# Kernel tuning notes

Measured on AMD Instinct MI355X. Metric: run time of the kernel, lower is better.

## Reference

```python
import jax, jax.numpy as jnp
import numpy as np

HID = 2048      # hidden_size
H = 16          # num query heads
KV = 4          # num kv heads
HD = HID // H   # head_dim = 128
THETA = 1000000.0
T = 2048        # tokens (single causal sequence)


def _rope(x, positions):
    # neox-style rotate-half RoPE over full head_dim. x: [T, h, HD]
    half = HD // 2
    inv_freq = THETA ** (-jnp.arange(half, dtype=jnp.float32) * 2.0 / HD)  # [half]
    freqs = positions.astype(jnp.float32)[:, None] * inv_freq              # [T, half]
    cos = jnp.cos(freqs)[:, None, :]
    sin = jnp.sin(freqs)[:, None, :]
    x1, x2 = x[..., :half], x[..., half:]
    return jnp.concatenate([x1 * cos - x2 * sin, x2 * cos + x1 * sin], axis=-1)


def setup_inputs() -> dict:
    key = jax.random.key(0)
    k1, k2, k3 = jax.random.split(key, 3)
    hidden_states = jax.random.normal(k1, (T, HID), jnp.float32) * 0.02
    w_qkv = jax.random.normal(k2, (HID, (H + 2 * KV) * HD), jnp.float32) * 0.02
    w_o = jax.random.normal(k3, (H * HD, HID), jnp.float32) * 0.02
    positions = jnp.arange(T, dtype=jnp.int32)
    return {"hidden_states": hidden_states, "w_qkv": w_qkv, "w_o": w_o,
            "positions": positions}


def reference(hidden_states, w_qkv, w_o, positions):
    q_size, kv_size = H * HD, KV * HD
    qkv = hidden_states @ w_qkv                                  # [T, q+2kv]
    q = qkv[:, :q_size].reshape(T, H, HD)
    k = qkv[:, q_size:q_size + kv_size].reshape(T, KV, HD)
    v = qkv[:, q_size + kv_size:].reshape(T, KV, HD)
    q = _rope(q, positions)
    k = _rope(k, positions)
    # GQA: expand kv heads to query heads
    group = H // KV
    k_e = jnp.repeat(k, group, axis=1)                           # [T, H, HD]
    v_e = jnp.repeat(v, group, axis=1)
    scale = HD ** -0.5
    scores = jnp.einsum('thd,shd->hts', q, k_e) * scale          # [H, T, T]
    causal = positions[:, None] >= positions[None, :]            # [T, T]
    scores = jnp.where(causal[None, :, :], scores, -1e30)
    attn = jax.nn.softmax(scores, axis=-1)
    o = jnp.einsum('hts,shd->thd', attn, v_e).reshape(T, H * HD)
    return o @ w_o
```

## Files before the change

### kernel.cpp

```cpp
#include <hip/hip_runtime.h>
#include <hip/hip_bf16.h>

#define T_LEN 2048
#define HID 2048
#define NH 16
#define NKV 4
#define HD 128
#define QKV_COLS 3072

typedef __attribute__((ext_vector_type(8))) short bf16x8;
typedef __attribute__((ext_vector_type(4))) float f32x4;

static __device__ __forceinline__ ushort f2bf(float f) {
  __hip_bfloat16 h = __float2bfloat16(f);
  return *reinterpret_cast<ushort*>(&h);
}
static __device__ __forceinline__ float bf2f(ushort u) {
  union { unsigned int i; float f; } v;
  v.i = ((unsigned int)u) << 16;
  return v.f;
}

static __device__ __forceinline__ void async_copy16(const ushort* g, ushort* l) {
  __builtin_amdgcn_global_load_lds(
      (const __attribute__((address_space(1))) unsigned int*)g,
      (__attribute__((address_space(3))) unsigned int*)l, 16, 0, 0);
}

__global__ __launch_bounds__(256) void prep(
    const float* __restrict__ hidden, ushort* __restrict__ hb,
    const float* __restrict__ w_qkv, ushort* __restrict__ wqkvT,
    const int* __restrict__ positions, float2* __restrict__ tbl,
    const float* __restrict__ w_o, ushort* __restrict__ woT) {
  __shared__ float t[64][65];
  const int b = blockIdx.x;
  const int tid = threadIdx.x;
  if (b < 4096) {
    int idx = (b * 256 + tid) * 4;
    float4 v = *(const float4*)(hidden + idx);
    ushort4 o;
    o.x = f2bf(v.x); o.y = f2bf(v.y); o.z = f2bf(v.z); o.w = f2bf(v.w);
    *(ushort4*)(hb + idx) = o;
  } else if (b < 5632) {
    const int tb = b - 4096;
    const int bk = (tb & 31) * 64, bn = (tb >> 5) * 64;
    const int c = tid & 63;
#pragma unroll
    for (int i = 0; i < 16; ++i) {
      int r = (tid >> 6) + i * 4;
      t[r][c] = w_qkv[(size_t)(bk + r) * QKV_COLS + bn + c];
    }
    __syncthreads();
#pragma unroll
    for (int i = 0; i < 16; ++i) {
      int r = (tid >> 6) + i * 4;
      wqkvT[(size_t)(bn + r) * HID + bk + c] = f2bf(t[c][r]);
    }
  } else if (b < 6144) {
    const int rb = b - 5632;
    const int tt = rb * 4 + (tid >> 6), j = tid & 63;
    double inv_freq = pow(1000000.0, -(double)(2 * j) / 128.0);
    double ang = (double)positions[tt] * inv_freq;
    double s, c2;
    sincos(ang, &s, &c2);
    tbl[(size_t)tt * 64 + j] = make_float2((float)c2, (float)s);
  } else {
    const int tb = b - 6144;
    const int bk = (tb & 31) * 64, bn = (tb >> 5) * 64;
    const int c = tid & 63;
#pragma unroll
    for (int i = 0; i < 16; ++i) {
      int r = (tid >> 6) + i * 4;
      t[r][c] = w_o[(size_t)(bk + r) * HID + bn + c];
    }
    __syncthreads();
#pragma unroll
    for (int i = 0; i < 16; ++i) {
      int r = (tid >> 6) + i * 4;
      woT[(size_t)(bn + r) * HID + bk + c] = f2bf(t[c][r]);
    }
  }
}

__global__ __launch_bounds__(256) void transpose_cast(
    const float* __restrict__ W, ushort* __restrict__ WT, int K, int N) {
  __shared__ float t[64][65];
  const int bk = blockIdx.x * 64, bn = blockIdx.y * 64;
  const int tid = threadIdx.x;
  const int c = tid & 63;
#pragma unroll
  for (int i = 0; i < 16; ++i) {
    int r = (tid >> 6) + i * 4;
    t[r][c] = W[(size_t)(bk + r) * N + bn + c];
  }
  __syncthreads();
#pragma unroll
  for (int i = 0; i < 16; ++i) {
    int r = (tid >> 6) + i * 4;
    WT[(size_t)(bn + r) * K + bk + c] = f2bf(t[c][r]);
  }
}

template <bool OUT_BF16>
__global__ __launch_bounds__(256, 3) void gemm_bt(
    const ushort* __restrict__ A, const ushort* __restrict__ BT,
    void* __restrict__ C, int M, int N, int K) {
  __shared__ __align__(16) ushort lds[2][1536 * 8];
  const int tid = threadIdx.x;
  const int bm = blockIdx.y * 64, bn = blockIdx.x * 128;
  const int wave = tid >> 6, lane = tid & 63;
  const int lr = lane & 15, lq = lane >> 4;
  const int wm = (wave & 1) * 32, wn = (wave >> 1) * 64;

  f32x4 acc[2][4];
#pragma unroll
  for (int i = 0; i < 2; ++i)
#pragma unroll
    for (int j = 0; j < 4; ++j) {
      acc[i][j][0] = 0.f; acc[i][j][1] = 0.f;
      acc[i][j][2] = 0.f; acc[i][j][3] = 0.f;
    }

  auto stage = [&](int k0, int buf) {
#pragma unroll
    for (int it = 0; it < 2; ++it) {
      int c = it * 256 + tid;
      int row = c >> 3, sl = c & 7, kc = sl ^ (row & 7);
      async_copy16(A + (size_t)(bm + row) * K + k0 + kc * 8, &lds[buf][c * 8]);
    }
#pragma unroll
    for (int it = 0; it < 4; ++it) {
      int c = it * 256 + tid;
      int row = c >> 3, sl = c & 7, kc = sl ^ (row & 7);
      async_copy16(BT + (size_t)(bn + row) * K + k0 + kc * 8,
                   &lds[buf][(512 + c) * 8]);
    }
  };

  stage(0, 0);
  __syncthreads();
  int cur = 0;
  for (int k0 = 0; k0 < K; k0 += 64) {
    if (k0 + 64 < K) stage(k0 + 64, cur ^ 1);
#pragma unroll
    for (int ks = 0; ks < 2; ++ks) {
      bf16x8 af[2], bfr[4];
#pragma unroll
      for (int mi = 0; mi < 2; ++mi) {
        int row = wm + mi * 16 + lr, kc = ks * 4 + lq;
        af[mi] = *(const bf16x8*)&lds[cur][(row * 8 + (kc ^ (row & 7))) * 8];
      }
#pragma unroll
      for (int ni = 0; ni < 4; ++ni) {
        int row = wn + ni * 16 + lr, kc = ks * 4 + lq;
        bfr[ni] =
            *(const bf16x8*)&lds[cur][(512 + row * 8 + (kc ^ (row & 7))) * 8];
      }
#pragma unroll
      for (int mi = 0; mi < 2; ++mi)
#pragma unroll
        for (int ni = 0; ni < 4; ++ni)
          acc[mi][ni] = __builtin_amdgcn_mfma_f32_16x16x32_bf16(
              af[mi], bfr[ni], acc[mi][ni], 0, 0, 0);
    }
    __syncthreads();
    cur ^= 1;
  }

#pragma unroll
  for (int mi = 0; mi < 2; ++mi)
#pragma unroll
    for (int ni = 0; ni < 4; ++ni)
#pragma unroll
      for (int r = 0; r < 4; ++r) {
        size_t row = bm + wm + mi * 16 + lq * 4 + r;
        size_t col = bn + wn + ni * 16 + lr;
        if (OUT_BF16)
          ((ushort*)C)[row * N + col] = f2bf(acc[mi][ni][r]);
        else
          ((float*)C)[row * N + col] = acc[mi][ni][r];
      }
}

__global__ __launch_bounds__(256, 3) void gemm_qkv(
    const ushort* __restrict__ A, const ushort* __restrict__ BT,
    ushort* __restrict__ qkvb, ushort* __restrict__ vt,
    const float2* __restrict__ tbl, int M, int N, int K) {
  __shared__ __align__(16) ushort lds[2][1536 * 8];
  const int tid = threadIdx.x;
  const int bm = blockIdx.y * 64, bn = blockIdx.x * 128;
  const int wave = tid >> 6, lane = tid & 63;
  const int lr = lane & 15, lq = lane >> 4;
  const int wm = (wave & 1) * 32, wn = (wave >> 1) * 64;

  f32x4 acc[2][4];
#pragma unroll
  for (int i = 0; i < 2; ++i)
#pragma unroll
    for (int j = 0; j < 4; ++j) {
      acc[i][j][0] = 0.f; acc[i][j][1] = 0.f;
      acc[i][j][2] = 0.f; acc[i][j][3] = 0.f;
    }

  auto stage = [&](int k0, int buf) {
#pragma unroll
    for (int it = 0; it < 2; ++it) {
      int c = it * 256 + tid;
      int row = c >> 3, sl = c & 7, kc = sl ^ (row & 7);
      async_copy16(A + (size_t)(bm + row) * K + k0 + kc * 8, &lds[buf][c * 8]);
    }
#pragma unroll
    for (int it = 0; it < 4; ++it) {
      int c = it * 256 + tid;
      int row = c >> 3, sl = c & 7, kc = sl ^ (row & 7);
      async_copy16(BT + (size_t)(bn + row) * K + k0 + kc * 8,
                   &lds[buf][(512 + c) * 8]);
    }
  };

  stage(0, 0);
  __syncthreads();
  int cur = 0;
  for (int k0 = 0; k0 < K; k0 += 64) {
    if (k0 + 64 < K) stage(k0 + 64, cur ^ 1);
#pragma unroll
    for (int ks = 0; ks < 2; ++ks) {
      bf16x8 af[2], bfr[4];
#pragma unroll
      for (int mi = 0; mi < 2; ++mi) {
        int row = wm + mi * 16 + lr, kc = ks * 4 + lq;
        af[mi] = *(const bf16x8*)&lds[cur][(row * 8 + (kc ^ (row & 7))) * 8];
      }
#pragma unroll
      for (int ni = 0; ni < 4; ++ni) {
        int row = wn + ni * 16 + lr, kc = ks * 4 + lq;
        bfr[ni] =
            *(const bf16x8*)&lds[cur][(512 + row * 8 + (kc ^ (row & 7))) * 8];
      }
#pragma unroll
      for (int mi = 0; mi < 2; ++mi)
#pragma unroll
        for (int ni = 0; ni < 4; ++ni)
          acc[mi][ni] = __builtin_amdgcn_mfma_f32_16x16x32_bf16(
              af[mi], bfr[ni], acc[mi][ni], 0, 0, 0);
    }
    __syncthreads();
    cur ^= 1;
  }

  const int head = bn >> 7;
  ushort* ep = &lds[0][0];
  if (head < 20) {
#pragma unroll
    for (int mi = 0; mi < 2; ++mi)
#pragma unroll
      for (int ni = 0; ni < 4; ++ni)
#pragma unroll
        for (int r = 0; r < 4; ++r)
          ep[(wm + mi * 16 + lq * 4 + r) * 130 + wn + ni * 16 + lr] =
              f2bf(acc[mi][ni][r]);
    __syncthreads();

    const float qs = (head < NH) ? 0.08838834764831845f : 1.0f;
#pragma unroll
    for (int it = 0; it < 16; ++it) {
      int idx = it * 256 + tid;
      int row = idx >> 6, j = idx & 63;
      float x1 = bf2f(ep[row * 130 + j]);
      float x2 = bf2f(ep[row * 130 + 64 + j]);
      float2 cs = tbl[(size_t)(bm + row) * 64 + j];
      qkvb[(size_t)(bm + row) * QKV_COLS + bn + j] =
          f2bf((x1 * cs.x - x2 * cs.y) * qs);
      qkvb[(size_t)(bm + row) * QKV_COLS + bn + 64 + j] =
          f2bf((x2 * cs.x + x1 * cs.y) * qs);
    }
  } else {
#pragma unroll
    for (int mi = 0; mi < 2; ++mi)
#pragma unroll
      for (int ni = 0; ni < 4; ++ni)
#pragma unroll
        for (int r = 0; r < 4; ++r)
          ep[(wm + mi * 16 + lq * 4 + r) * 130 + wn + ni * 16 + lr] =
              f2bf(acc[mi][ni][r]);
    __syncthreads();

    const int vd0 = bn - 2560;
#pragma unroll
    for (int it = 0; it < 8; ++it) {
      int idx = it * 256 + tid;
      int vd = idx >> 4, tg = (idx & 15) * 4;
      ushort4 w;
      w.x = ep[(tg + 0) * 130 + vd];
      w.y = ep[(tg + 1) * 130 + vd];
      w.z = ep[(tg + 2) * 130 + vd];
      w.w = ep[(tg + 3) * 130 + vd];
      *(ushort4*)&vt[(size_t)(vd0 + vd) * T_LEN + bm + tg] = w;
    }
  }
}

__global__ __launch_bounds__(256, 3) void attn_mfma(
    const ushort* __restrict__ qkv, const ushort* __restrict__ vt,
    ushort* __restrict__ o, ushort* __restrict__ partials,
    float* __restrict__ ml) {
  int qt, h, k_begin, k_end, slot = -1;
  {
    const int i = blockIdx.x;
    int c = 0, nc = 1;
    if (i < 64) {
      qt = 11 - (i >> 4); h = i & 15;
    } else if (i < 448) {
      int j = i - 64;
      qt = 23 - (j >> 5);
      int rem = j & 31;
      h = rem >> 1; c = rem & 1; nc = 2;
      slot = ((qt - 12) * 16 + h) * 2 + c;
    } else if (i < 832) {
      int j = i - 448;
      qt = 31 - (j / 48);
      int rem = j % 48;
      h = rem / 3; c = rem % 3; nc = 3;
      slot = 384 + ((qt - 24) * 16 + h) * 3 + c;
    } else {
      int j = i - 832;
      qt = 7 - (j >> 4); h = j & 15;
    }
    const int n = qt + 1;
    k_begin = (n * c) / nc;
    k_end = (n * (c + 1)) / nc;
  }
  const int kh = h >> 2;
  const int tid = threadIdx.x;
  const int wave = tid >> 6, lane = tid & 63;
  const int lr = lane & 15, lq = lane >> 4;
  const int wq = wave >> 1, ws = wave & 1;

  __shared__ __align__(16) ushort KsL[1024 * 8];
  __shared__ __align__(16) ushort VtsL[1024 * 8];
  __shared__ __align__(16) ushort Ps[8 * 67 * 8];
  __shared__ float l_sh[64][2];

  bf16x8 qf[2][4];
  {
    const ushort* qbase =
        qkv + (size_t)(qt * 64 + wq * 32 + lr) * QKV_COLS + h * HD + lq * 8;
#pragma unroll
    for (int mi = 0; mi < 2; ++mi)
#pragma unroll
      for (int kk = 0; kk < 4; ++kk)
        qf[mi][kk] = *(const bf16x8*)(qbase + (size_t)mi * 16 * QKV_COLS + kk * 32);
  }

  float l_part[2][4];
#pragma unroll
  for (int mi = 0; mi < 2; ++mi)
#pragma unroll
    for (int r = 0; r < 4; ++r) l_part[mi][r] = 0.f;
  f32x4 o_acc[4][2];
#pragma unroll
  for (int qi = 0; qi < 4; ++qi)
#pragma unroll
    for (int di = 0; di < 2; ++di) {
      o_acc[qi][di][0] = 0.f; o_acc[qi][di][1] = 0.f;
      o_acc[qi][di][2] = 0.f; o_acc[qi][di][3] = 0.f;
    }

  for (int kt = k_begin; kt < k_end; ++kt) {
    __syncthreads();

    {
      const ushort* kbase = qkv + 2048 + kh * HD;
#pragma unroll
      for (int it = 0; it < 4; ++it) {
        int c = it * 256 + tid;
        int s = c >> 4, sl = c & 15, dg = sl ^ (s & 15);
        async_copy16(kbase + (size_t)(kt * 64 + s) * QKV_COLS + dg * 8,
                     &KsL[c * 8]);
      }
    }
    {
      const ushort* vbase = vt + (size_t)(kh * HD) * T_LEN + kt * 64;
#pragma unroll
      for (int it = 0; it < 4; ++it) {
        int c = it * 256 + tid;
        int d = c >> 3, sl = c & 7, sc = sl ^ (d & 7);
        async_copy16(vbase + (size_t)d * T_LEN + sc * 8, &VtsL[c * 8]);
      }
    }
    __syncthreads();

    f32x4 s_acc[2][2];
#pragma unroll
    for (int mi = 0; mi < 2; ++mi)
#pragma unroll
      for (int ni = 0; ni < 2; ++ni) {
        s_acc[mi][ni][0] = 0.f; s_acc[mi][ni][1] = 0.f;
        s_acc[mi][ni][2] = 0.f; s_acc[mi][ni][3] = 0.f;
      }
    __builtin_amdgcn_s_setprio(1);
#pragma unroll
    for (int kk = 0; kk < 4; ++kk) {
      bf16x8 kf[2];
#pragma unroll
      for (int ni = 0; ni < 2; ++ni) {
        int s = ws * 32 + ni * 16 + lr;
        kf[ni] = *(const bf16x8*)&KsL[(s * 16 + ((kk * 4 + lq) ^ (s & 15))) * 8];
      }
#pragma unroll
      for (int mi = 0; mi < 2; ++mi)
#pragma unroll
        for (int ni = 0; ni < 2; ++ni)
          s_acc[mi][ni] = __builtin_amdgcn_mfma_f32_16x16x32_bf16(
              qf[mi][kk], kf[ni], s_acc[mi][ni], 0, 0, 0);
    }
    __builtin_amdgcn_s_setprio(0);

    if (kt == qt) {
#pragma unroll
      for (int mi = 0; mi < 2; ++mi)
#pragma unroll
        for (int ni = 0; ni < 2; ++ni)
#pragma unroll
          for (int r = 0; r < 4; ++r)
            if (ws * 32 + ni * 16 + lr > wq * 32 + mi * 16 + lq * 4 + r)
              s_acc[mi][ni][r] = -1e30f;
    }

#pragma unroll
    for (int mi = 0; mi < 2; ++mi)
#pragma unroll
      for (int ni = 0; ni < 2; ++ni)
#pragma unroll
        for (int r = 0; r < 4; ++r) {
          float p = __expf(s_acc[mi][ni][r]);
          l_part[mi][r] += p;
          int s = ws * 32 + ni * 16 + lr;
          int q = wq * 32 + mi * 16 + lq * 4 + r;
          Ps[((s >> 3) * 67 + q) * 8 + (s & 7)] = f2bf(p);
        }
    __syncthreads();

    __builtin_amdgcn_s_setprio(1);
#pragma unroll
    for (int ss = 0; ss < 2; ++ss) {
      bf16x8 vf[2];
#pragma unroll
      for (int di = 0; di < 2; ++di) {
        int d = wave * 32 + di * 16 + lr, sc = ss * 4 + lq;
        vf[di] = *(const bf16x8*)&VtsL[(d * 8 + (sc ^ (d & 7))) * 8];
      }
#pragma unroll
      for (int qi = 0; qi < 4; ++qi) {
        bf16x8 pf = *(const bf16x8*)&Ps[((ss * 4 + lq) * 67 + qi * 16 + lr) * 8];
#pragma unroll
        for (int di = 0; di < 2; ++di)
          o_acc[qi][di] = __builtin_amdgcn_mfma_f32_16x16x32_bf16(
              pf, vf[di], o_acc[qi][di], 0, 0, 0);
      }
    }
    __builtin_amdgcn_s_setprio(0);
  }

#pragma unroll
  for (int mi = 0; mi < 2; ++mi)
#pragma unroll
    for (int r = 0; r < 4; ++r) {
      float v = l_part[mi][r];
#pragma unroll
      for (int off = 1; off < 16; off <<= 1) v += __shfl_xor(v, off, 16);
      l_part[mi][r] = v;
    }
  if (lr == 0) {
#pragma unroll
    for (int mi = 0; mi < 2; ++mi)
#pragma unroll
      for (int r = 0; r < 4; ++r)
        l_sh[wq * 32 + mi * 16 + lq * 4 + r][ws] = l_part[mi][r];
  }
  __syncthreads();

  if (slot < 0) {
    ushort* ob = o + (size_t)(qt * 64) * (NH * HD) + h * HD + wave * 32;
#pragma unroll
    for (int qi = 0; qi < 4; ++qi)
#pragma unroll
      for (int r = 0; r < 4; ++r) {
        int q = qi * 16 + lq * 4 + r;
        float inv = 1.f / (l_sh[q][0] + l_sh[q][1]);
#pragma unroll
        for (int di = 0; di < 2; ++di)
          ob[(size_t)q * (NH * HD) + di * 16 + lr] =
              f2bf(o_acc[qi][di][r] * inv);
      }
  } else {
    ushort* pb = partials + (size_t)slot * 64 * HD + wave * 32;
#pragma unroll
    for (int qi = 0; qi < 4; ++qi)
#pragma unroll
      for (int r = 0; r < 4; ++r) {
        int q = qi * 16 + lq * 4 + r;
#pragma unroll
        for (int di = 0; di < 2; ++di)
          pb[(size_t)q * HD + di * 16 + lr] = f2bf(o_acc[qi][di][r]);
      }
    if (tid < 64) ml[(size_t)slot * 64 + tid] = l_sh[tid][0] + l_sh[tid][1];
  }
}

__global__ __launch_bounds__(256) void attn_reduce(
    const ushort* __restrict__ partials, const float* __restrict__ ml,
    ushort* __restrict__ o) {
  const int bi = blockIdx.x;
  int qt, h, base, cnt;
  if (bi < 192) {
    qt = 12 + (bi >> 4); h = bi & 15;
    base = ((qt - 12) * 16 + h) * 2; cnt = 2;
  } else {
    int k = bi - 192;
    qt = 24 + (k >> 4); h = k & 15;
    base = 384 + ((qt - 24) * 16 + h) * 3; cnt = 3;
  }
  const int tid = threadIdx.x;
  const int row = tid >> 2;
  const int dq = (tid & 3) * 32;

  float lsum = 0.f;
  for (int c = 0; c < cnt; ++c) lsum += ml[(size_t)(base + c) * 64 + row];
  const float inv = 1.f / lsum;

  float accf[32];
#pragma unroll
  for (int k = 0; k < 32; ++k) accf[k] = 0.f;
  for (int c = 0; c < cnt; ++c) {
    const ushort* p = partials + ((size_t)(base + c) * 64 + row) * HD + dq;
#pragma unroll
    for (int v = 0; v < 4; ++v) {
      bf16x8 a = *(const bf16x8*)(p + v * 8);
#pragma unroll
      for (int k = 0; k < 8; ++k) accf[v * 8 + k] += bf2f((ushort)a[k]);
    }
  }
  ushort* ob = o + (size_t)(qt * 64 + row) * (NH * HD) + h * HD + dq;
#pragma unroll
  for (int v = 0; v < 4; ++v) {
    bf16x8 w;
#pragma unroll
    for (int k = 0; k < 8; ++k)
      w[k] = (short)f2bf(accf[v * 8 + k] * inv);
    *(bf16x8*)(ob + v * 8) = w;
  }
}

extern "C" void kernel_launch(void* const* d_in, const int* in_sizes, int n_in,
                              void* d_out, int out_size, void* d_ws,
                              size_t ws_size, hipStream_t stream) {
  const float* hidden = (const float*)d_in[0];
  const float* w_qkv  = (const float*)d_in[1];
  const float* w_o    = (const float*)d_in[2];
  const int* positions = (const int*)d_in[3];
  float* out = (float*)d_out;

  ushort* ws = (ushort*)d_ws;
  ushort* hb    = ws;
  ushort* wqkvT = ws + 4194304;
  ushort* qkvb  = wqkvT + 6291456;
  ushort* vtb   = qkvb + 6291456;
  float*  mlb   = (float*)(vtb + 1048576);
  float2* tbl   = (float2*)(mlb + 49152);
  ushort* wsend = (ushort*)(tbl + 131072);
  ushort* ob       = hb;
  ushort* partials = wqkvT;

  const size_t need_bytes = (18448384ull + 4194304ull) * 2;
  const bool fast = ws_size >= need_bytes;
  ushort* woT = fast ? wsend : wqkvT;

  prep<<<fast ? 7168 : 6144, 256, 0, stream>>>(
      hidden, hb, w_qkv, wqkvT, positions, tbl, w_o, woT);

  gemm_qkv<<<dim3(QKV_COLS / 128, T_LEN / 64), 256, 0, stream>>>(
      hb, wqkvT, qkvb, vtb, tbl, T_LEN, QKV_COLS, HID);

  attn_mfma<<<960, 256, 0, stream>>>(qkvb, vtb, ob, partials, mlb);
  attn_reduce<<<320, 256, 0, stream>>>(partials, mlb, ob);

  if (!fast)
    transpose_cast<<<dim3(HID / 64, HID / 64), 256, 0, stream>>>(
        w_o, woT, HID, HID);

  gemm_bt<false><<<dim3(HID / 128, T_LEN / 64), 256, 0, stream>>>(
      ob, woT, out, T_LEN, HID, NH * HD);
}
```

Measured before the change: 197.9 us.

## Fuse split-K attention reduction into attention kernel via atomic counters

Removes the separate attn_reduce launch. Each split block now writes its partial result, bumps a per-group atomic counter, and the last block to finish sums the partials and writes the normalized output. The counters are zeroed in the prep kernel and stored in a new workspace region. This trades one launch and its tail for threadfence/atomic overhead and a serialized reduce at the end of the last block in each group.

```diff
diff --git a/kernel.cpp b/kernel.cpp
--- a/kernel.cpp
+++ b/kernel.cpp
@@ -31,11 +31,13 @@
     const float* __restrict__ hidden, ushort* __restrict__ hb,
     const float* __restrict__ w_qkv, ushort* __restrict__ wqkvT,
     const int* __restrict__ positions, float2* __restrict__ tbl,
-    const float* __restrict__ w_o, ushort* __restrict__ woT) {
+    const float* __restrict__ w_o, ushort* __restrict__ woT,
+    unsigned int* __restrict__ cnt) {
   __shared__ float t[64][65];
   const int b = blockIdx.x;
   const int tid = threadIdx.x;
   if (b < 4096) {
+    if (b == 0) { cnt[tid] = 0u; cnt[tid + 256] = 0u; }
     int idx = (b * 256 + tid) * 4;
     float4 v = *(const float4*)(hidden + idx);
     ushort4 o;
@@ -303,11 +305,11 @@
 __global__ __launch_bounds__(256, 3) void attn_mfma(
     const ushort* __restrict__ qkv, const ushort* __restrict__ vt,
     ushort* __restrict__ o, ushort* __restrict__ partials,
-    float* __restrict__ ml) {
-  int qt, h, k_begin, k_end, slot = -1;
+    float* __restrict__ ml, unsigned int* __restrict__ cnt) {
+  int qt, h, k_begin, k_end, slot = -1, sbase = 0, grp = -1, nc = 1;
   {
     const int i = blockIdx.x;
-    int c = 0, nc = 1;
+    int c = 0;
     if (i < 64) {
       qt = 11 - (i >> 4); h = i & 15;
     } else if (i < 448) {
@@ -315,13 +317,17 @@
       qt = 23 - (j >> 5);
       int rem = j & 31;
       h = rem >> 1; c = rem & 1; nc = 2;
-      slot = ((qt - 12) * 16 + h) * 2 + c;
+      grp = (qt - 12) * 16 + h;
+      sbase = grp * 2;
+      slot = sbase + c;
     } else if (i < 832) {
       int j = i - 448;
       qt = 31 - (j / 48);
       int rem = j % 48;
       h = rem / 3; c = rem % 3; nc = 3;
-      slot = 384 + ((qt - 24) * 16 + h) * 3 + c;
+      grp = 192 + (qt - 24) * 16 + h;
+      sbase = 384 + ((qt - 24) * 16 + h) * 3;
+      slot = sbase + c;
     } else {
       int j = i - 832;
       qt = 7 - (j >> 4); h = j & 15;
@@ -340,6 +346,7 @@
   __shared__ __align__(16) ushort VtsL[1024 * 8];
   __shared__ __align__(16) ushort Ps[8 * 67 * 8];
   __shared__ float l_sh[64][2];
+  __shared__ unsigned int done_sh;
 
   bf16x8 qf[2][4];
   {
@@ -505,50 +512,43 @@
           pb[(size_t)q * HD + di * 16 + lr] = f2bf(o_acc[qi][di][r]);
       }
     if (tid < 64) ml[(size_t)slot * 64 + tid] = l_sh[tid][0] + l_sh[tid][1];
-  }
-}
-
-__global__ __launch_bounds__(256) void attn_reduce(
-    const ushort* __restrict__ partials, const float* __restrict__ ml,
-    ushort* __restrict__ o) {
-  const int bi = blockIdx.x;
-  int qt, h, base, cnt;
-  if (bi < 192) {
-    qt = 12 + (bi >> 4); h = bi & 15;
-    base = ((qt - 12) * 16 + h) * 2; cnt = 2;
-  } else {
-    int k = bi - 192;
-    qt = 24 + (k >> 4); h = k & 15;
-    base = 384 + ((qt - 24) * 16 + h) * 3; cnt = 3;
-  }
-  const int tid = threadIdx.x;
-  const int row = tid >> 2;
-  const int dq = (tid & 3) * 32;
-
-  float lsum = 0.f;
-  for (int c = 0; c < cnt; ++c) lsum += ml[(size_t)(base + c) * 64 + row];
-  const float inv = 1.f / lsum;
-
-  float accf[32];
-#pragma unroll
-  for (int k = 0; k < 32; ++k) accf[k] = 0.f;
-  for (int c = 0; c < cnt; ++c) {
-    const ushort* p = partials + ((size_t)(base + c) * 64 + row) * HD + dq;
-#pragma unroll
-    for (int v = 0; v < 4; ++v) {
-      bf16x8 a = *(const bf16x8*)(p + v * 8);
-#pragma unroll
-      for (int k = 0; k < 8; ++k) accf[v * 8 + k] += bf2f((ushort)a[k]);
-    }
-  }
-  ushort* ob = o + (size_t)(qt * 64 + row) * (NH * HD) + h * HD + dq;
-#pragma unroll
-  for (int v = 0; v < 4; ++v) {
-    bf16x8 w;
-#pragma unroll
-    for (int k = 0; k < 8; ++k)
-      w[k] = (short)f2bf(accf[v * 8 + k] * inv);
-    *(bf16x8*)(ob + v * 8) = w;
+
+    __threadfence();
+    __syncthreads();
+    if (tid == 0) done_sh = atomicAdd(&cnt[grp], 1u);
+    __syncthreads();
+    if (done_sh == (unsigned)(nc - 1)) {
+      __threadfence();
+      const int row = tid >> 2;
+      const int dq = (tid & 3) * 32;
+      float lsum = 0.f;
+      for (int c2 = 0; c2 < nc; ++c2)
+        lsum += ml[(size_t)(sbase + c2) * 64 + row];
+      const float inv = 1.f / lsum;
+
+      float accf[32];
+#pragma unroll
+      for (int k = 0; k < 32; ++k) accf[k] = 0.f;
+      for (int c2 = 0; c2 < nc; ++c2) {
+        const ushort* p =
+            partials + ((size_t)(sbase + c2) * 64 + row) * HD + dq;
+#pragma unroll
+        for (int v = 0; v < 4; ++v) {
+          bf16x8 a = *(const bf16x8*)(p + v * 8);
+#pragma unroll
+          for (int k = 0; k < 8; ++k) accf[v * 8 + k] += bf2f((ushort)a[k]);
+        }
+      }
+      ushort* ob = o + (size_t)(qt * 64 + row) * (NH * HD) + h * HD + dq;
+#pragma unroll
+      for (int v = 0; v < 4; ++v) {
+        bf16x8 w;
+#pragma unroll
+        for (int k = 0; k < 8; ++k)
+          w[k] = (short)f2bf(accf[v * 8 + k] * inv);
+        *(bf16x8*)(ob + v * 8) = w;
+      }
+    }
   }
 }
 
@@ -568,22 +568,22 @@
   ushort* vtb   = qkvb + 6291456;
   float*  mlb   = (float*)(vtb + 1048576);
   float2* tbl   = (float2*)(mlb + 49152);
-  ushort* wsend = (ushort*)(tbl + 131072);
+  unsigned int* cntb = (unsigned int*)(tbl + 131072);
+  ushort* wsend = (ushort*)(cntb + 512);
   ushort* ob       = hb;
   ushort* partials = wqkvT;
 
-  const size_t need_bytes = (18448384ull + 4194304ull) * 2;
+  const size_t need_bytes = (18449408ull + 4194304ull) * 2;
   const bool fast = ws_size >= need_bytes;
   ushort* woT = fast ? wsend : wqkvT;
 
   prep<<<fast ? 7168 : 6144, 256, 0, stream>>>(
-      hidden, hb, w_qkv, wqkvT, positions, tbl, w_o, woT);
+      hidden, hb, w_qkv, wqkvT, positions, tbl, w_o, woT, cntb);
 
   gemm_qkv<<<dim3(QKV_COLS / 128, T_LEN / 64), 256, 0, stream>>>(
       hb, wqkvT, qkvb, vtb, tbl, T_LEN, QKV_COLS, HID);
 
-  attn_mfma<<<960, 256, 0, stream>>>(qkvb, vtb, ob, partials, mlb);
-  attn_reduce<<<320, 256, 0, stream>>>(partials, mlb, ob);
+  attn_mfma<<<960, 256, 0, stream>>>(qkvb, vtb, ob, partials, mlb, cntb);
 
   if (!fast)
     transpose_cast<<<dim3(HID / 64, HID / 64), 256, 0, stream>>>(
```

After: 360.8 us. 1.82x slower.

## Fuse attention partial reduction into output GEMM via cooperative grid sync

Applied to the files above, without the earlier changes.

Merges the attn_reduce kernel into the output-projection GEMM, launched as a cooperative kernel: the first 320 blocks do the split-KV reduction, the whole grid syncs, then every block runs the GEMM tile. This removes one kernel launch and the gap between the two kernels. In exchange it adds a grid-wide barrier, and it requires all 512 blocks to be co-resident. If the cooperative launch fails, the code falls back to the separate kernels.

```diff
diff --git a/kernel.cpp b/kernel.cpp
--- a/kernel.cpp
+++ b/kernel.cpp
@@ -1,5 +1,8 @@
 #include <hip/hip_runtime.h>
 #include <hip/hip_bf16.h>
+#include <hip/hip_cooperative_groups.h>
+
+namespace cg = cooperative_groups;
 
 #define T_LEN 2048
 #define HID 2048
@@ -101,13 +104,12 @@
   }
 }
 
-template <bool OUT_BF16>
-__global__ __launch_bounds__(256, 3) void gemm_bt(
+static __device__ __forceinline__ void gemm_bt_body(
     const ushort* __restrict__ A, const ushort* __restrict__ BT,
-    void* __restrict__ C, int M, int N, int K) {
-  __shared__ __align__(16) ushort lds[2][1536 * 8];
-  const int tid = threadIdx.x;
-  const int bm = blockIdx.y * 64, bn = blockIdx.x * 128;
+    float* __restrict__ C, int M, int N, int K,
+    int bx, int by, int tid, ushort* lds0, ushort* lds1) {
+  ushort* ldsb[2] = {lds0, lds1};
+  const int bm = by * 64, bn = bx * 128;
   const int wave = tid >> 6, lane = tid & 63;
   const int lr = lane & 15, lq = lane >> 4;
   const int wm = (wave & 1) * 32, wn = (wave >> 1) * 64;
@@ -126,14 +128,15 @@
     for (int it = 0; it < 2; ++it) {
       int c = it * 256 + tid;
       int row = c >> 3, sl = c & 7, kc = sl ^ (row & 7);
-      async_copy16(A + (size_t)(bm + row) * K + k0 + kc * 8, &lds[buf][c * 8]);
+      async_copy16(A + (size_t)(bm + row) * K + k0 + kc * 8,
+                   &ldsb[buf][c * 8]);
     }
 #pragma unroll
     for (int it = 0; it < 4; ++it) {
       int c = it * 256 + tid;
       int row = c >> 3, sl = c & 7, kc = sl ^ (row & 7);
       async_copy16(BT + (size_t)(bn + row) * K + k0 + kc * 8,
-                   &lds[buf][(512 + c) * 8]);
+                   &ldsb[buf][(512 + c) * 8]);
     }
   };
 
@@ -148,13 +151,13 @@
 #pragma unroll
       for (int mi = 0; mi < 2; ++mi) {
         int row = wm + mi * 16 + lr, kc = ks * 4 + lq;
-        af[mi] = *(const bf16x8*)&lds[cur][(row * 8 + (kc ^ (row & 7))) * 8];
+        af[mi] = *(const bf16x8*)&ldsb[cur][(row * 8 + (kc ^ (row & 7))) * 8];
       }
 #pragma unroll
       for (int ni = 0; ni < 4; ++ni) {
         int row = wn + ni * 16 + lr, kc = ks * 4 + lq;
         bfr[ni] =
-            *(const bf16x8*)&lds[cur][(512 + row * 8 + (kc ^ (row & 7))) * 8];
+            *(const bf16x8*)&ldsb[cur][(512 + row * 8 + (kc ^ (row & 7))) * 8];
       }
 #pragma unroll
       for (int mi = 0; mi < 2; ++mi)
@@ -175,11 +178,77 @@
       for (int r = 0; r < 4; ++r) {
         size_t row = bm + wm + mi * 16 + lq * 4 + r;
         size_t col = bn + wn + ni * 16 + lr;
-        if (OUT_BF16)
-          ((ushort*)C)[row * N + col] = f2bf(acc[mi][ni][r]);
-        else
-          ((float*)C)[row * N + col] = acc[mi][ni][r];
-      }
+        C[row * N + col] = acc[mi][ni][r];
+      }
+}
+
+__global__ __launch_bounds__(256, 3) void gemm_bt(
+    const ushort* __restrict__ A, const ushort* __restrict__ BT,
+    float* __restrict__ C, int M, int N, int K) {
+  __shared__ __align__(16) ushort lds[2][1536 * 8];
+  gemm_bt_body(A, BT, C, M, N, K, blockIdx.x, blockIdx.y, threadIdx.x,
+               lds[0], lds[1]);
+}
+
+static __device__ __forceinline__ void attn_reduce_body(
+    const ushort* __restrict__ partials, const float* __restrict__ ml,
+    ushort* __restrict__ o, int bi, int tid) {
+  int qt, h, base, cnt;
+  if (bi < 192) {
+    qt = 12 + (bi >> 4); h = bi & 15;
+    base = ((qt - 12) * 16 + h) * 2; cnt = 2;
+  } else {
+    int k = bi - 192;
+    qt = 24 + (k >> 4); h = k & 15;
+    base = 384 + ((qt - 24) * 16 + h) * 3; cnt = 3;
+  }
+  const int row = tid >> 2;
+  const int dq = (tid & 3) * 32;
+
+  float lsum = 0.f;
+  for (int c = 0; c < cnt; ++c) lsum += ml[(size_t)(base + c) * 64 + row];
+  const float inv = 1.f / lsum;
+
+  float accf[32];
+#pragma unroll
+  for (int k = 0; k < 32; ++k) accf[k] = 0.f;
+  for (int c = 0; c < cnt; ++c) {
+    const ushort* p = partials + ((size_t)(base + c) * 64 + row) * HD + dq;
+#pragma unroll
+    for (int v = 0; v < 4; ++v) {
+      bf16x8 a = *(const bf16x8*)(p + v * 8);
+#pragma unroll
+      for (int k = 0; k < 8; ++k) accf[v * 8 + k] += bf2f((ushort)a[k]);
+    }
+  }
+  ushort* ob = o + (size_t)(qt * 64 + row) * (NH * HD) + h * HD + dq;
+#pragma unroll
+  for (int v = 0; v < 4; ++v) {
+    bf16x8 w;
+#pragma unroll
+    for (int k = 0; k < 8; ++k)
+      w[k] = (short)f2bf(accf[v * 8 + k] * inv);
+    *(bf16x8*)(ob + v * 8) = w;
+  }
+}
+
+__global__ __launch_bounds__(256) void attn_reduce(
+    const ushort* __restrict__ partials, const float* __restrict__ ml,
+    ushort* __restrict__ o) {
+  attn_reduce_body(partials, ml, o, blockIdx.x, threadIdx.x);
+}
+
+__global__ __launch_bounds__(256, 3) void gemm_bt_red(
+    const ushort* __restrict__ partials, const float* __restrict__ ml,
+    ushort* __restrict__ ob, const ushort* __restrict__ BT,
+    float* __restrict__ C, int M, int N, int K) {
+  __shared__ __align__(16) ushort lds[2][1536 * 8];
+  const int flat = blockIdx.y * gridDim.x + blockIdx.x;
+  if (flat < 320)
+    attn_reduce_body(partials, ml, ob, flat, threadIdx.x);
+  cg::this_grid().sync();
+  gemm_bt_body(ob, BT, C, M, N, K, blockIdx.x, blockIdx.y, threadIdx.x,
+               lds[0], lds[1]);
 }
 
 __global__ __launch_bounds__(256, 3) void gemm_qkv(
@@ -508,50 +577,6 @@
   }
 }
 
-__global__ __launch_bounds__(256) void attn_reduce(
-    const ushort* __restrict__ partials, const float* __restrict__ ml,
-    ushort* __restrict__ o) {
-  const int bi = blockIdx.x;
-  int qt, h, base, cnt;
-  if (bi < 192) {
-    qt = 12 + (bi >> 4); h = bi & 15;
-    base = ((qt - 12) * 16 + h) * 2; cnt = 2;
-  } else {
-    int k = bi - 192;
-    qt = 24 + (k >> 4); h = k & 15;
-    base = 384 + ((qt - 24) * 16 + h) * 3; cnt = 3;
-  }
-  const int tid = threadIdx.x;
-  const int row = tid >> 2;
-  const int dq = (tid & 3) * 32;
-
-  float lsum = 0.f;
-  for (int c = 0; c < cnt; ++c) lsum += ml[(size_t)(base + c) * 64 + row];
-  const float inv = 1.f / lsum;
-
-  float accf[32];
-#pragma unroll
-  for (int k = 0; k < 32; ++k) accf[k] = 0.f;
-  for (int c = 0; c < cnt; ++c) {
-    const ushort* p = partials + ((size_t)(base + c) * 64 + row) * HD + dq;
-#pragma unroll
-    for (int v = 0; v < 4; ++v) {
-      bf16x8 a = *(const bf16x8*)(p + v * 8);
-#pragma unroll
-      for (int k = 0; k < 8; ++k) accf[v * 8 + k] += bf2f((ushort)a[k]);
-    }
-  }
-  ushort* ob = o + (size_t)(qt * 64 + row) * (NH * HD) + h * HD + dq;
-#pragma unroll
-  for (int v = 0; v < 4; ++v) {
-    bf16x8 w;
-#pragma unroll
-    for (int k = 0; k < 8; ++k)
-      w[k] = (short)f2bf(accf[v * 8 + k] * inv);
-    *(bf16x8*)(ob + v * 8) = w;
-  }
-}
-
 extern "C" void kernel_launch(void* const* d_in, const int* in_sizes, int n_in,
                               void* d_out, int out_size, void* d_ws,
                               size_t ws_size, hipStream_t stream) {
@@ -583,12 +608,29 @@
       hb, wqkvT, qkvb, vtb, tbl, T_LEN, QKV_COLS, HID);
 
   attn_mfma<<<960, 256, 0, stream>>>(qkvb, vtb, ob, partials, mlb);
-  attn_reduce<<<320, 256, 0, stream>>>(partials, mlb, ob);
-
-  if (!fast)
-    transpose_cast<<<dim3(HID / 64, HID / 64), 256, 0, stream>>>(
-        w_o, woT, HID, HID);
-
-  gemm_bt<false><<<dim3(HID / 128, T_LEN / 64), 256, 0, stream>>>(
-      ob, woT, out, T_LEN, HID, NH * HD);
-}
+
+  bool fused_done = false;
+  if (fast) {
+    const ushort* pa = partials;
+    const float*  mla = mlb;
+    ushort* oba = ob;
+    const ushort* bta = woT;
+    float* ca = out;
+    int M = T_LEN, N = HID, K = NH * HD;
+    void* args[] = {(void*)&pa, (void*)&mla, (void*)&oba,
+                    (void*)&bta, (void*)&ca, (void*)&M, (void*)&N, (void*)&K};
+    hipError_t e = hipLaunchCooperativeKernel(
+        reinterpret_cast<void*>(gemm_bt_red),
+        dim3(HID / 128, T_LEN / 64), dim3(256), args, 0, stream);
+    fused_done = (e == hipSuccess);
+  }
+
+  if (!fused_done) {
+    attn_reduce<<<320, 256, 0, stream>>>(partials, mlb, ob);
+    if (!fast)
+      transpose_cast<<<dim3(HID / 64, HID / 64), 256, 0, stream>>>(
+          w_o, woT, HID, HID);
+    gemm_bt<<<dim3(HID / 128, T_LEN / 64), 256, 0, stream>>>(
+        ob, woT, out, T_LEN, HID, NH * HD);
+  }
+}
```

After: 286.2 us. 1.45x slower.

## Double attention query tile to 128 rows with 512-thread blocks sharing K/V

Applied to the files above, without the earlier changes.

The attention kernel now processes 128 query rows per block with 8 waves instead of 64 rows with 4 waves. Each K/V tile loaded into LDS is therefore reused by twice as many queries, halving global K/V traffic per query. The causal mask, work split, partial-buffer layout and reduce kernel are remapped to the new 128-row tiles. In exchange there are fewer, larger blocks, which may balance worse across CUs. The launch-bounds hint now asks for 6 waves per EU, which tightens the register budget and may cause spills.

```diff
diff --git a/kernel.cpp b/kernel.cpp
--- a/kernel.cpp
+++ b/kernel.cpp
@@ -300,33 +300,30 @@
   }
 }
 
-__global__ __launch_bounds__(256, 3) void attn_mfma(
+__global__ __launch_bounds__(512, 6) void attn_mfma(
     const ushort* __restrict__ qkv, const ushort* __restrict__ vt,
     ushort* __restrict__ o, ushort* __restrict__ partials,
     float* __restrict__ ml) {
-  int qt, h, k_begin, k_end, slot = -1;
+  int qt2, h, k_begin, k_end, slot = -1;
   {
     const int i = blockIdx.x;
     int c = 0, nc = 1;
-    if (i < 64) {
-      qt = 11 - (i >> 4); h = i & 15;
-    } else if (i < 448) {
-      int j = i - 64;
-      qt = 23 - (j >> 5);
+    if (i < 192) {
+      qt2 = 15 - (i / 48);
+      int rem = i % 48;
+      h = rem / 3; c = rem % 3; nc = 3;
+      slot = ((qt2 - 12) * 16 + h) * 3 + c;
+    } else if (i < 384) {
+      int j = i - 192;
+      qt2 = 11 - (j >> 5);
       int rem = j & 31;
       h = rem >> 1; c = rem & 1; nc = 2;
-      slot = ((qt - 12) * 16 + h) * 2 + c;
-    } else if (i < 832) {
-      int j = i - 448;
-      qt = 31 - (j / 48);
-      int rem = j % 48;
-      h = rem / 3; c = rem % 3; nc = 3;
-      slot = 384 + ((qt - 24) * 16 + h) * 3 + c;
+      slot = 192 + ((qt2 - 6) * 16 + h) * 2 + c;
     } else {
-      int j = i - 832;
-      qt = 7 - (j >> 4); h = j & 15;
-    }
-    const int n = qt + 1;
+      int j = i - 384;
+      qt2 = 5 - (j >> 4); h = j & 15;
+    }
+    const int n = 2 * qt2 + 2;
     k_begin = (n * c) / nc;
     k_end = (n * (c + 1)) / nc;
   }
@@ -335,16 +332,17 @@
   const int wave = tid >> 6, lane = tid & 63;
   const int lr = lane & 15, lq = lane >> 4;
   const int wq = wave >> 1, ws = wave & 1;
+  const int qh = wave >> 2, wd = wave & 3;
 
   __shared__ __align__(16) ushort KsL[1024 * 8];
   __shared__ __align__(16) ushort VtsL[1024 * 8];
-  __shared__ __align__(16) ushort Ps[8 * 67 * 8];
-  __shared__ float l_sh[64][2];
+  __shared__ __align__(16) ushort Ps[8 * 131 * 8];
+  __shared__ float l_sh[128][2];
 
   bf16x8 qf[2][4];
   {
     const ushort* qbase =
-        qkv + (size_t)(qt * 64 + wq * 32 + lr) * QKV_COLS + h * HD + lq * 8;
+        qkv + (size_t)(qt2 * 128 + wq * 32 + lr) * QKV_COLS + h * HD + lq * 8;
 #pragma unroll
     for (int mi = 0; mi < 2; ++mi)
 #pragma unroll
@@ -372,20 +370,20 @@
     {
       const ushort* kbase = qkv + 2048 + kh * HD;
 #pragma unroll
-      for (int it = 0; it < 4; ++it) {
-        int c = it * 256 + tid;
-        int s = c >> 4, sl = c & 15, dg = sl ^ (s & 15);
+      for (int it = 0; it < 2; ++it) {
+        int c2 = it * 512 + tid;
+        int s = c2 >> 4, sl = c2 & 15, dg = sl ^ (s & 15);
         async_copy16(kbase + (size_t)(kt * 64 + s) * QKV_COLS + dg * 8,
-                     &KsL[c * 8]);
+                     &KsL[c2 * 8]);
       }
     }
     {
       const ushort* vbase = vt + (size_t)(kh * HD) * T_LEN + kt * 64;
 #pragma unroll
-      for (int it = 0; it < 4; ++it) {
-        int c = it * 256 + tid;
-        int d = c >> 3, sl = c & 7, sc = sl ^ (d & 7);
-        async_copy16(vbase + (size_t)d * T_LEN + sc * 8, &VtsL[c * 8]);
+      for (int it = 0; it < 2; ++it) {
+        int c2 = it * 512 + tid;
+        int d = c2 >> 3, sl = c2 & 7, sc = sl ^ (d & 7);
+        async_copy16(vbase + (size_t)d * T_LEN + sc * 8, &VtsL[c2 * 8]);
       }
     }
     __syncthreads();
@@ -416,15 +414,17 @@
     }
     __builtin_amdgcn_s_setprio(0);
 
-    if (kt == qt) {
+    if (kt >= 2 * qt2) {
 #pragma unroll
       for (int mi = 0; mi < 2; ++mi)
 #pragma unroll
         for (int ni = 0; ni < 2; ++ni)
 #pragma unroll
-          for (int r = 0; r < 4; ++r)
-            if (ws * 32 + ni * 16 + lr > wq * 32 + mi * 16 + lq * 4 + r)
+          for (int r = 0; r < 4; ++r) {
+            int sg = kt * 64 - qt2 * 128 + ws * 32 + ni * 16 + lr;
+            if (sg > wq * 32 + mi * 16 + lq * 4 + r)
               s_acc[mi][ni][r] = -1e30f;
+          }
     }
 
 #pragma unroll
@@ -437,7 +437,7 @@
           l_part[mi][r] += p;
           int s = ws * 32 + ni * 16 + lr;
           int q = wq * 32 + mi * 16 + lq * 4 + r;
-          Ps[((s >> 3) * 67 + q) * 8 + (s & 7)] = f2bf(p);
+          Ps[((s >> 3) * 131 + q) * 8 + (s & 7)] = f2bf(p);
         }
     __syncthreads();
 
@@ -447,12 +447,13 @@
       bf16x8 vf[2];
 #pragma unroll
       for (int di = 0; di < 2; ++di) {
-        int d = wave * 32 + di * 16 + lr, sc = ss * 4 + lq;
+        int d = wd * 32 + di * 16 + lr, sc = ss * 4 + lq;
         vf[di] = *(const bf16x8*)&VtsL[(d * 8 + (sc ^ (d & 7))) * 8];
       }
 #pragma unroll
       for (int qi = 0; qi < 4; ++qi) {
-        bf16x8 pf = *(const bf16x8*)&Ps[((ss * 4 + lq) * 67 + qi * 16 + lr) * 8];
+        bf16x8 pf = *(const bf16x8*)
+            &Ps[((ss * 4 + lq) * 131 + qh * 64 + qi * 16 + lr) * 8];
 #pragma unroll
         for (int di = 0; di < 2; ++di)
           o_acc[qi][di] = __builtin_amdgcn_mfma_f32_16x16x32_bf16(
@@ -481,12 +482,12 @@
   __syncthreads();
 
   if (slot < 0) {
-    ushort* ob = o + (size_t)(qt * 64) * (NH * HD) + h * HD + wave * 32;
+    ushort* ob = o + (size_t)(qt2 * 128) * (NH * HD) + h * HD + wd * 32;
 #pragma unroll
     for (int qi = 0; qi < 4; ++qi)
 #pragma unroll
       for (int r = 0; r < 4; ++r) {
-        int q = qi * 16 + lq * 4 + r;
+        int q = qh * 64 + qi * 16 + lq * 4 + r;
         float inv = 1.f / (l_sh[q][0] + l_sh[q][1]);
 #pragma unroll
         for (int di = 0; di < 2; ++di)
@@ -494,17 +495,17 @@
               f2bf(o_acc[qi][di][r] * inv);
       }
   } else {
-    ushort* pb = partials + (size_t)slot * 64 * HD + wave * 32;
+    ushort* pb = partials + (size_t)slot * 128 * HD + wd * 32;
 #pragma unroll
     for (int qi = 0; qi < 4; ++qi)
 #pragma unroll
       for (int r = 0; r < 4; ++r) {
-        int q = qi * 16 + lq * 4 + r;
+        int q = qh * 64 + qi * 16 + lq * 4 + r;
 #pragma unroll
         for (int di = 0; di < 2; ++di)
           pb[(size_t)q * HD + di * 16 + lr] = f2bf(o_acc[qi][di][r]);
       }
-    if (tid < 64) ml[(size_t)slot * 64 + tid] = l_sh[tid][0] + l_sh[tid][1];
+    if (tid < 128) ml[(size_t)slot * 128 + tid] = l_sh[tid][0] + l_sh[tid][1];
   }
 }
 
@@ -512,38 +513,38 @@
     const ushort* __restrict__ partials, const float* __restrict__ ml,
     ushort* __restrict__ o) {
   const int bi = blockIdx.x;
-  int qt, h, base, cnt;
-  if (bi < 192) {
-    qt = 12 + (bi >> 4); h = bi & 15;
-    base = ((qt - 12) * 16 + h) * 2; cnt = 2;
+  int qt2, h, base, cnt;
+  if (bi < 96) {
+    qt2 = 6 + (bi >> 4); h = bi & 15;
+    base = 192 + ((qt2 - 6) * 16 + h) * 2; cnt = 2;
   } else {
-    int k = bi - 192;
-    qt = 24 + (k >> 4); h = k & 15;
-    base = 384 + ((qt - 24) * 16 + h) * 3; cnt = 3;
+    int k = bi - 96;
+    qt2 = 12 + (k >> 4); h = k & 15;
+    base = ((qt2 - 12) * 16 + h) * 3; cnt = 3;
   }
   const int tid = threadIdx.x;
-  const int row = tid >> 2;
-  const int dq = (tid & 3) * 32;
+  const int row = tid >> 1;
+  const int dq = (tid & 1) * 64;
 
   float lsum = 0.f;
-  for (int c = 0; c < cnt; ++c) lsum += ml[(size_t)(base + c) * 64 + row];
+  for (int c = 0; c < cnt; ++c) lsum += ml[(size_t)(base + c) * 128 + row];
   const float inv = 1.f / lsum;
 
-  float accf[32];
-#pragma unroll
-  for (int k = 0; k < 32; ++k) accf[k] = 0.f;
+  float accf[64];
+#pragma unroll
+  for (int k = 0; k < 64; ++k) accf[k] = 0.f;
   for (int c = 0; c < cnt; ++c) {
-    const ushort* p = partials + ((size_t)(base + c) * 64 + row) * HD + dq;
-#pragma unroll
-    for (int v = 0; v < 4; ++v) {
+    const ushort* p = partials + ((size_t)(base + c) * 128 + row) * HD + dq;
+#pragma unroll
+    for (int v = 0; v < 8; ++v) {
       bf16x8 a = *(const bf16x8*)(p + v * 8);
 #pragma unroll
       for (int k = 0; k < 8; ++k) accf[v * 8 + k] += bf2f((ushort)a[k]);
     }
   }
-  ushort* ob = o + (size_t)(qt * 64 + row) * (NH * HD) + h * HD + dq;
-#pragma unroll
-  for (int v = 0; v < 4; ++v) {
+  ushort* ob = o + (size_t)(qt2 * 128 + row) * (NH * HD) + h * HD + dq;
+#pragma unroll
+  for (int v = 0; v < 8; ++v) {
     bf16x8 w;
 #pragma unroll
     for (int k = 0; k < 8; ++k)
@@ -582,8 +583,8 @@
   gemm_qkv<<<dim3(QKV_COLS / 128, T_LEN / 64), 256, 0, stream>>>(
       hb, wqkvT, qkvb, vtb, tbl, T_LEN, QKV_COLS, HID);
 
-  attn_mfma<<<960, 256, 0, stream>>>(qkvb, vtb, ob, partials, mlb);
-  attn_reduce<<<320, 256, 0, stream>>>(partials, mlb, ob);
+  attn_mfma<<<480, 512, 0, stream>>>(qkvb, vtb, ob, partials, mlb);
+  attn_reduce<<<160, 256, 0, stream>>>(partials, mlb, ob);
 
   if (!fast)
     transpose_cast<<<dim3(HID / 64, HID / 64), 256, 0, stream>>>(
```

Result: slower. 293.3 us (+48.3%).
